# Kernel optimization log

Measured on AMD Instinct MI355X. Metric: run time of the kernel, lower is better.

Reference implementation:

```python
import jax, jax.numpy as jnp
import numpy as np

N = 50000
IN_F = 200
OUT_F = 200
NRELA = 200
E1 = 400000
E2 = 100000
ALPHA = 0.2  # leakyrelu slope


def setup_inputs() -> dict:
    key = jax.random.key(0)
    ks = jax.random.split(key, 9)
    xav = float(np.sqrt(2.0 / (OUT_F + 2 * IN_F + NRELA))) * 1.414
    return {
        "x": jax.random.normal(ks[0], (N, IN_F), dtype=jnp.float32),
        "edge": jax.random.randint(ks[1], (2, E1), 0, N, dtype=jnp.int32),
        "edge_embed": jax.random.normal(ks[2], (E1, NRELA), dtype=jnp.float32),
        "edge_list_nhop": jax.random.randint(ks[3], (2, E2), 0, N, dtype=jnp.int32),
        "edge_embed_nhop": jax.random.normal(ks[4], (E2, NRELA), dtype=jnp.float32),
        "a": jax.random.normal(ks[5], (OUT_F, 2 * IN_F + NRELA), dtype=jnp.float32) * xav,
        "a_2": jax.random.normal(ks[6], (1, OUT_F), dtype=jnp.float32) * float(np.sqrt(2.0 / (1 + OUT_F))) * 1.414,
        "mlp_w": jax.random.normal(ks[7], (1, OUT_F), dtype=jnp.float32) * float(np.sqrt(1.0 / OUT_F)),
        "mlp_b": jnp.zeros((1,), dtype=jnp.float32),
    }


def reference(x, edge, edge_embed, edge_list_nhop, edge_embed_nhop, a, a_2, mlp_w, mlp_b):
    # concat 1-hop and n-hop edges: e [2,E], emb [E,nrela]
    e = jnp.concatenate([edge, edge_list_nhop], axis=1)
    emb = jnp.concatenate([edge_embed, edge_embed_nhop], axis=0)
    src = e[0]
    dst = e[1]
    n_edges = emb.shape[0]
    # edge_h: [E, 2*in + nrela]
    edge_h = jnp.concatenate([x[src], x[dst], emb], axis=1)
    # edge_m = a @ edge_h.T, kept as [E, out]
    edge_m = edge_h @ a.T
    # powers = -leakyrelu(a_2 @ edge_m): [E]
    powers = -jax.nn.leaky_relu(edge_m @ a_2[0], ALPHA)
    # inline MLP: tanh(Linear(edge_m)) -> [E]
    y = jnp.tanh(edge_m @ mlp_w[0] + mlp_b[0])
    powers = powers * y / n_edges
    edge_e = jnp.exp(powers)  # [E]
    n = x.shape[0]
    # segment-sum over source nodes (sparse.sum over dim=1 of coo[src,dst,:])
    e_rowsum = jax.ops.segment_sum(edge_e, src, num_segments=n)[:, None]  # [N,1]
    e_rowsum = jnp.where(e_rowsum == 0.0, 1e-12, e_rowsum)
    # weighted scatter-add of edge messages
    edge_w = edge_e[:, None] * edge_m  # [E, out]
    h_prime = jax.ops.segment_sum(edge_w, src, num_segments=n)  # [N, out]
    h_prime = h_prime / e_rowsum
    return jax.nn.elu(h_prime)  # concat=True
```

## Files before the change

### kernel.cpp

```cpp
#include <hip/hip_runtime.h>
#include <math.h>

#define NN    50000
#define FDIM  200
#define E1N   400000
#define E2N   100000
#define EN    500000

typedef __attribute__((ext_vector_type(8))) short short8;
typedef __attribute__((ext_vector_type(4))) float f32x4;

#define VALL_OFF   0
#define WALL_OFF   608
#define SCAL_OFF   1216
#define XS_OFF     201216
#define RS_OFF     10201216
#define CNT_OFF    10251216
#define FILL_OFF   10301216
#define INCL_OFF   10351216
#define BSUM_OFF   10401216
#define SORT_OFF   10401472
#define XB_OFF     10901472
#define AB_OFF     15901472
#define TB_OFF     15961472

static __device__ __forceinline__ unsigned short f2bf(float f) {
    unsigned int u = __float_as_uint(f);
    unsigned int r = (u + 0x7fffu + ((u >> 16) & 1u)) >> 16;
    return (unsigned short)r;
}

__global__ void k_coeffs(const float* __restrict__ a, const float* __restrict__ a2,
                         const float* __restrict__ mlpw,
                         float* __restrict__ vall, float* __restrict__ wall) {
    int k = blockIdx.x * blockDim.x + threadIdx.x;
    if (k >= 600) return;
    float v = 0.f, w = 0.f;
    for (int o = 0; o < FDIM; ++o) {
        float av = a[o * 600 + k];
        v += a2[o] * av;
        w += mlpw[o] * av;
    }
    vall[k] = v;
    wall[k] = w;
}

__global__ __launch_bounds__(256) void k_node_scal(const float* __restrict__ x,
                                                   const float* __restrict__ vall,
                                                   const float* __restrict__ wall,
                                                   float* __restrict__ scal) {
    __shared__ float sv[1200];
    int tid = threadIdx.x;
    for (int i = tid; i < 1200; i += 256) sv[i] = (i < 600) ? vall[i] : wall[i - 600];
    __syncthreads();
    int lane = tid & 63;
    int n = blockIdx.x * 4 + (tid >> 6);
    float ps = 0.f, pd = 0.f, qs = 0.f, qd = 0.f;
    for (int k = lane; k < FDIM; k += 64) {
        float xv = x[(size_t)n * FDIM + k];
        ps += xv * sv[k];
        pd += xv * sv[200 + k];
        qs += xv * sv[600 + k];
        qd += xv * sv[800 + k];
    }
    #pragma unroll
    for (int off = 32; off > 0; off >>= 1) {
        ps += __shfl_xor(ps, off);
        pd += __shfl_xor(pd, off);
        qs += __shfl_xor(qs, off);
        qd += __shfl_xor(qd, off);
    }
    if (lane == 0) {
        float4 r = make_float4(ps, pd, qs, qd);
        *(float4*)(scal + (size_t)n * 4) = r;
    }
}

__global__ __launch_bounds__(256) void k_cvt(const float* __restrict__ src,
                                             unsigned short* __restrict__ dst, int n4) {
    int i = blockIdx.x * 256 + threadIdx.x;
    if (i >= n4) return;
    float4 v = *(const float4*)(src + (size_t)i * 4);
    ushort4 o;
    o.x = f2bf(v.x); o.y = f2bf(v.y); o.z = f2bf(v.z); o.w = f2bf(v.w);
    *(ushort4*)(dst + (size_t)i * 4) = o;
}

__global__ __launch_bounds__(256) void k_hist(const int* __restrict__ edge,
                                              const int* __restrict__ edgenh,
                                              int* __restrict__ counts) {
    int g = blockIdx.x * 256 + threadIdx.x;
    if (g >= EN) return;
    int s = (g < E1N) ? edge[g] : edgenh[g - E1N];
    atomicAdd(counts + s, 1);
}

__global__ __launch_bounds__(256) void k_scan1(const int* __restrict__ counts,
                                               int* __restrict__ incl,
                                               int* __restrict__ bsums) {
    __shared__ int tmp[256];
    int g = blockIdx.x * 256 + threadIdx.x;
    int v = (g < NN) ? counts[g] : 0;
    tmp[threadIdx.x] = v;
    __syncthreads();
    for (int off = 1; off < 256; off <<= 1) {
        int t = (threadIdx.x >= off) ? tmp[threadIdx.x - off] : 0;
        __syncthreads();
        tmp[threadIdx.x] += t;
        __syncthreads();
    }
    if (g < NN) incl[g] = tmp[threadIdx.x];
    if (threadIdx.x == 255) bsums[blockIdx.x] = tmp[255];
}

__global__ __launch_bounds__(256) void k_scan2(int* __restrict__ bsums, int nb) {
    __shared__ int tmp[256];
    int v = (threadIdx.x < nb) ? bsums[threadIdx.x] : 0;
    tmp[threadIdx.x] = v;
    __syncthreads();
    for (int off = 1; off < 256; off <<= 1) {
        int t = (threadIdx.x >= off) ? tmp[threadIdx.x - off] : 0;
        __syncthreads();
        tmp[threadIdx.x] += t;
        __syncthreads();
    }
    if (threadIdx.x < nb) bsums[threadIdx.x] = tmp[threadIdx.x] - v;
}

__global__ __launch_bounds__(256) void k_scan3(const int* __restrict__ counts,
                                               int* __restrict__ incl,
                                               const int* __restrict__ bsums) {
    int g = blockIdx.x * 256 + threadIdx.x;
    if (g >= NN) return;
    incl[g] = incl[g] - counts[g] + bsums[blockIdx.x];
}

__global__ __launch_bounds__(256) void k_scatter(const int* __restrict__ edge,
                                                 const int* __restrict__ edgenh,
                                                 const int* __restrict__ offs,
                                                 int* __restrict__ fill,
                                                 int* __restrict__ sorted) {
    int g = blockIdx.x * 256 + threadIdx.x;
    if (g >= EN) return;
    int s = (g < E1N) ? edge[g] : edgenh[g - E1N];
    int pos = offs[s] + atomicAdd(fill + s, 1);
    sorted[pos] = g;
}

__global__ __launch_bounds__(256) void k_csr(const int* __restrict__ sorted,
                                             const int* __restrict__ offs,
                                             const int* __restrict__ counts,
                                             const int* __restrict__ edge,
                                             const int* __restrict__ edgenh,
                                             const float* __restrict__ ee,
                                             const float* __restrict__ eenh,
                                             const float* __restrict__ x,
                                             const float* __restrict__ vall,
                                             const float* __restrict__ wall,
                                             const float* __restrict__ scal,
                                             const float* __restrict__ mlpb,
                                             float* __restrict__ rowsum,
                                             unsigned short* __restrict__ Tb) {
    int tid = threadIdx.x, lane = tid & 63;
    int n = blockIdx.x * 4 + (tid >> 6);
    float4 v3 = make_float4(0, 0, 0, 0), w3 = v3;
    if (lane < 50) {
        v3 = *(const float4*)(vall + 400 + lane * 4);
        w3 = *(const float4*)(wall + 400 + lane * 4);
    }
    float4 sc_n = *(const float4*)(scal + (size_t)n * 4);
    float mb = mlpb[0];
    int beg = offs[n], cnt = counts[n];
    float accx0 = 0, accx1 = 0, accx2 = 0, accx3 = 0;
    float acce0 = 0, acce1 = 0, acce2 = 0, acce3 = 0;
    float rs = 0.f;
    for (int i = 0; i < cnt; ++i) {
        int e = sorted[beg + i];
        int d;
        const float* erow;
        if (e < E1N) { d = edge[E1N + e]; erow = ee + (size_t)e * FDIM; }
        else { int e2 = e - E1N; d = edgenh[E2N + e2]; erow = eenh + (size_t)e2 * FDIM; }
        float4 ev = make_float4(0, 0, 0, 0), xv = ev;
        if (lane < 50) {
            ev = *(const float4*)(erow + lane * 4);
            xv = *(const float4*)(x + (size_t)d * FDIM + lane * 4);
        }
        float pe = ev.x * v3.x + ev.y * v3.y + ev.z * v3.z + ev.w * v3.w;
        float qe = ev.x * w3.x + ev.y * w3.y + ev.z * w3.z + ev.w * w3.w;
        #pragma unroll
        for (int off = 32; off > 0; off >>= 1) {
            pe += __shfl_xor(pe, off);
            qe += __shfl_xor(qe, off);
        }
        float4 sd = *(const float4*)(scal + (size_t)d * 4);
        float z1 = sc_n.x + sd.y + pe;
        float z2 = sc_n.z + sd.w + qe + mb;
        float l = z1 > 0.f ? z1 : 0.2f * z1;
        float wgt = expf((-l) * tanhf(z2) * (1.0f / (float)EN));
        rs += wgt;
        accx0 += wgt * xv.x; accx1 += wgt * xv.y; accx2 += wgt * xv.z; accx3 += wgt * xv.w;
        acce0 += wgt * ev.x; acce1 += wgt * ev.y; acce2 += wgt * ev.z; acce3 += wgt * ev.w;
    }
    if (lane == 0) rowsum[n] = rs;
    if (lane < 50) {
        ushort4 o1, o2;
        o1.x = f2bf(accx0); o1.y = f2bf(accx1); o1.z = f2bf(accx2); o1.w = f2bf(accx3);
        o2.x = f2bf(acce0); o2.y = f2bf(acce1); o2.z = f2bf(acce2); o2.w = f2bf(acce3);
        *(ushort4*)(Tb + (size_t)n * 400 + lane * 4) = o1;
        *(ushort4*)(Tb + (size_t)n * 400 + 200 + lane * 4) = o2;
    }
}

template <int KPAD, int KREAL, int LDA, int LDB, bool FINAL>
__global__ __launch_bounds__(256) void k_mfma(const unsigned short* __restrict__ A,
                                              const unsigned short* __restrict__ B,
                                              const float* __restrict__ Xs,
                                              const float* __restrict__ rowsum,
                                              float* __restrict__ C) {
    __shared__ unsigned short Al[64][40];
    __shared__ unsigned short Bl[64][40];
    int tid = threadIdx.x, w = tid >> 6, lane = tid & 63;
    int bx = blockIdx.x, by = blockIdx.y;
    f32x4 acc[4] = {};
    int r = tid >> 2, c = tid & 3;
    for (int k0 = 0; k0 < KPAD; k0 += 32) {
        int gk = k0 + c * 8;
        uint4 av = make_uint4(0, 0, 0, 0), bv = av;
        int arow = by * 64 + r;
        if (arow < NN && gk < KREAL)
            av = *(const uint4*)(A + (size_t)arow * LDA + gk);
        int brow = bx * 64 + r;
        if (brow < 200 && gk < KREAL)
            bv = *(const uint4*)(B + (size_t)brow * LDB + gk);
        *(uint4*)&Al[r][c * 8] = av;
        *(uint4*)&Bl[r][c * 8] = bv;
        __syncthreads();
        short8 af = *(short8*)&Al[w * 16 + (lane & 15)][(lane >> 4) * 8];
        #pragma unroll
        for (int ct = 0; ct < 4; ++ct) {
            short8 bf = *(short8*)&Bl[ct * 16 + (lane & 15)][(lane >> 4) * 8];
            acc[ct] = __builtin_amdgcn_mfma_f32_16x16x32_bf16(af, bf, acc[ct], 0, 0, 0);
        }
        __syncthreads();
    }
    #pragma unroll
    for (int ct = 0; ct < 4; ++ct) {
        #pragma unroll
        for (int rr = 0; rr < 4; ++rr) {
            int grow = by * 64 + w * 16 + (lane >> 4) * 4 + rr;
            int gcol = bx * 64 + ct * 16 + (lane & 15);
            if (grow < NN && gcol < 200) {
                float v = acc[ct][rr];
                if (FINAL) {
                    float rsv = rowsum[grow];
                    float o;
                    if (rsv == 0.f) o = 0.f;
                    else {
                        float h = Xs[(size_t)grow * 200 + gcol] + v / rsv;
                        o = h > 0.f ? h : expm1f(h);
                    }
                    C[(size_t)grow * 200 + gcol] = o;
                } else {
                    C[(size_t)grow * 200 + gcol] = v;
                }
            }
        }
    }
}

extern "C" void kernel_launch(void* const* d_in, const int* in_sizes, int n_in,
                              void* d_out, int out_size, void* d_ws, size_t ws_size,
                              hipStream_t stream) {
    const float* x      = (const float*)d_in[0];
    const int*   edge   = (const int*)d_in[1];
    const float* ee     = (const float*)d_in[2];
    const int*   edgenh = (const int*)d_in[3];
    const float* eenh   = (const float*)d_in[4];
    const float* a      = (const float*)d_in[5];
    const float* a2     = (const float*)d_in[6];
    const float* mlpw   = (const float*)d_in[7];
    const float* mlpb   = (const float*)d_in[8];

    float* ws = (float*)d_ws;
    float* vall   = ws + VALL_OFF;
    float* wall   = ws + WALL_OFF;
    float* scal   = ws + SCAL_OFF;
    float* Xs     = ws + XS_OFF;
    float* rowsum = ws + RS_OFF;
    int*   counts = (int*)(ws + CNT_OFF);
    int*   fill   = (int*)(ws + FILL_OFF);
    int*   incl   = (int*)(ws + INCL_OFF);
    int*   bsums  = (int*)(ws + BSUM_OFF);
    int*   sorted = (int*)(ws + SORT_OFF);
    unsigned short* xb = (unsigned short*)(ws + XB_OFF);
    unsigned short* ab = (unsigned short*)(ws + AB_OFF);
    unsigned short* Tb = (unsigned short*)(ws + TB_OFF);

    hipMemsetAsync(counts, 0, (size_t)(2 * NN) * sizeof(int), stream);

    k_coeffs<<<3, 256, 0, stream>>>(a, a2, mlpw, vall, wall);
    k_node_scal<<<NN / 4, 256, 0, stream>>>(x, vall, wall, scal);

    k_cvt<<<(NN * FDIM / 4 + 255) / 256, 256, 0, stream>>>(x, xb, NN * FDIM / 4);
    k_cvt<<<(200 * 600 / 4 + 255) / 256, 256, 0, stream>>>(a, ab, 200 * 600 / 4);

    k_hist<<<(EN + 255) / 256, 256, 0, stream>>>(edge, edgenh, counts);
    int nb = (NN + 255) / 256;
    k_scan1<<<nb, 256, 0, stream>>>(counts, incl, bsums);
    k_scan2<<<1, 256, 0, stream>>>(bsums, nb);
    k_scan3<<<nb, 256, 0, stream>>>(counts, incl, bsums);
    k_scatter<<<(EN + 255) / 256, 256, 0, stream>>>(edge, edgenh, incl, fill, sorted);

    dim3 gg(4, (NN + 63) / 64);
    k_mfma<224, 200, 200, 600, false><<<gg, 256, 0, stream>>>(xb, ab, nullptr, nullptr, Xs);

    k_csr<<<NN / 4, 256, 0, stream>>>(sorted, incl, counts, edge, edgenh, ee, eenh,
                                      x, vall, wall, scal, mlpb, rowsum, Tb);

    k_mfma<416, 400, 400, 600, true><<<gg, 256, 0, stream>>>(Tb, ab + 200, Xs, rowsum,
                                                             (float*)d_out);
}
```

Baseline: 821.9 us.

## Fuse two GEMMs into one K-concatenated GEMM and streamline CSR gather

Normalises the aggregated features by rowsum inside the CSR kernel, then computes the output with a single MFMA GEMM over the concatenated [x | T_src | T_emb] K dimension. This removes the intermediate fp32 Xs buffer and its write and read. Other changes: the bf16 conversion of x is fused into the node-scalar kernel, the CSR gather reads bf16 x, the destination is stored alongside the edge id in the sorted array, the next edge record is prefetched, and fast exp/rcp replace tanhf and expf. In exchange, the gathered neighbor features and normalised sums are rounded to bf16 and the fast transcendentals lose some accuracy.

```diff
diff --git a/kernel.cpp b/kernel.cpp
--- a/kernel.cpp
+++ b/kernel.cpp
@@ -13,21 +13,23 @@
 #define VALL_OFF   0
 #define WALL_OFF   608
 #define SCAL_OFF   1216
-#define XS_OFF     201216
-#define RS_OFF     10201216
-#define CNT_OFF    10251216
-#define FILL_OFF   10301216
-#define INCL_OFF   10351216
-#define BSUM_OFF   10401216
-#define SORT_OFF   10401472
-#define XB_OFF     10901472
-#define AB_OFF     15901472
-#define TB_OFF     15961472
+#define RS_OFF     201216
+#define CNT_OFF    251216
+#define FILL_OFF   301216
+#define INCL_OFF   351216
+#define BSUM_OFF   401216
+#define SORT_OFF   401472
+#define XB_OFF     1401472
+#define AB_OFF     6401472
+#define TSB_OFF    6461472
 
 static __device__ __forceinline__ unsigned short f2bf(float f) {
     unsigned int u = __float_as_uint(f);
     unsigned int r = (u + 0x7fffu + ((u >> 16) & 1u)) >> 16;
     return (unsigned short)r;
+}
+static __device__ __forceinline__ float bf2f(unsigned short s) {
+    return __uint_as_float((unsigned int)s << 16);
 }
 
 __global__ void k_coeffs(const float* __restrict__ a, const float* __restrict__ a2,
@@ -48,7 +50,8 @@
 __global__ __launch_bounds__(256) void k_node_scal(const float* __restrict__ x,
                                                    const float* __restrict__ vall,
                                                    const float* __restrict__ wall,
-                                                   float* __restrict__ scal) {
+                                                   float* __restrict__ scal,
+                                                   unsigned short* __restrict__ xb) {
     __shared__ float sv[1200];
     int tid = threadIdx.x;
     for (int i = tid; i < 1200; i += 256) sv[i] = (i < 600) ? vall[i] : wall[i - 600];
@@ -56,12 +59,19 @@
     int lane = tid & 63;
     int n = blockIdx.x * 4 + (tid >> 6);
     float ps = 0.f, pd = 0.f, qs = 0.f, qd = 0.f;
-    for (int k = lane; k < FDIM; k += 64) {
-        float xv = x[(size_t)n * FDIM + k];
-        ps += xv * sv[k];
-        pd += xv * sv[200 + k];
-        qs += xv * sv[600 + k];
-        qd += xv * sv[800 + k];
+    if (lane < 50) {
+        float4 xv = *(const float4*)(x + (size_t)n * FDIM + lane * 4);
+        float4 v1 = *(const float4*)(sv + lane * 4);
+        float4 v2 = *(const float4*)(sv + 200 + lane * 4);
+        float4 w1 = *(const float4*)(sv + 600 + lane * 4);
+        float4 w2 = *(const float4*)(sv + 800 + lane * 4);
+        ps = xv.x * v1.x + xv.y * v1.y + xv.z * v1.z + xv.w * v1.w;
+        pd = xv.x * v2.x + xv.y * v2.y + xv.z * v2.z + xv.w * v2.w;
+        qs = xv.x * w1.x + xv.y * w1.y + xv.z * w1.z + xv.w * w1.w;
+        qd = xv.x * w2.x + xv.y * w2.y + xv.z * w2.z + xv.w * w2.w;
+        ushort4 o;
+        o.x = f2bf(xv.x); o.y = f2bf(xv.y); o.z = f2bf(xv.z); o.w = f2bf(xv.w);
+        *(ushort4*)(xb + (size_t)n * FDIM + lane * 4) = o;
     }
     #pragma unroll
     for (int off = 32; off > 0; off >>= 1) {
@@ -129,38 +139,40 @@
 
 __global__ __launch_bounds__(256) void k_scan3(const int* __restrict__ counts,
                                                int* __restrict__ incl,
-                                               const int* __restrict__ bsums) {
+                                               const int* __restrict__ bsums,
+                                               int* __restrict__ fill) {
     int g = blockIdx.x * 256 + threadIdx.x;
     if (g >= NN) return;
-    incl[g] = incl[g] - counts[g] + bsums[blockIdx.x];
+    int v = incl[g] - counts[g] + bsums[blockIdx.x];
+    incl[g] = v;
+    fill[g] = v;
 }
 
 __global__ __launch_bounds__(256) void k_scatter(const int* __restrict__ edge,
                                                  const int* __restrict__ edgenh,
-                                                 const int* __restrict__ offs,
                                                  int* __restrict__ fill,
-                                                 int* __restrict__ sorted) {
+                                                 int2* __restrict__ sorted2) {
     int g = blockIdx.x * 256 + threadIdx.x;
     if (g >= EN) return;
-    int s = (g < E1N) ? edge[g] : edgenh[g - E1N];
-    int pos = offs[s] + atomicAdd(fill + s, 1);
-    sorted[pos] = g;
-}
-
-__global__ __launch_bounds__(256) void k_csr(const int* __restrict__ sorted,
+    int s, d;
+    if (g < E1N) { s = edge[g]; d = edge[E1N + g]; }
+    else { s = edgenh[g - E1N]; d = edgenh[E2N + (g - E1N)]; }
+    int pos = atomicAdd(fill + s, 1);
+    sorted2[pos] = make_int2(g, d);
+}
+
+__global__ __launch_bounds__(256) void k_csr(const int2* __restrict__ sorted2,
                                              const int* __restrict__ offs,
                                              const int* __restrict__ counts,
-                                             const int* __restrict__ edge,
-                                             const int* __restrict__ edgenh,
                                              const float* __restrict__ ee,
                                              const float* __restrict__ eenh,
-                                             const float* __restrict__ x,
+                                             const unsigned short* __restrict__ xb,
                                              const float* __restrict__ vall,
                                              const float* __restrict__ wall,
                                              const float* __restrict__ scal,
                                              const float* __restrict__ mlpb,
                                              float* __restrict__ rowsum,
-                                             unsigned short* __restrict__ Tb) {
+                                             unsigned short* __restrict__ Tsb) {
     int tid = threadIdx.x, lane = tid & 63;
     int n = blockIdx.x * 4 + (tid >> 6);
     float4 v3 = make_float4(0, 0, 0, 0), w3 = v3;
@@ -174,16 +186,17 @@
     float accx0 = 0, accx1 = 0, accx2 = 0, accx3 = 0;
     float acce0 = 0, acce1 = 0, acce2 = 0, acce3 = 0;
     float rs = 0.f;
+    int2 ed = (cnt > 0) ? sorted2[beg] : make_int2(0, 0);
     for (int i = 0; i < cnt; ++i) {
-        int e = sorted[beg + i];
-        int d;
-        const float* erow;
-        if (e < E1N) { d = edge[E1N + e]; erow = ee + (size_t)e * FDIM; }
-        else { int e2 = e - E1N; d = edgenh[E2N + e2]; erow = eenh + (size_t)e2 * FDIM; }
+        int2 ed_n = (i + 1 < cnt) ? sorted2[beg + i + 1] : ed;
+        int e = ed.x, d = ed.y;
+        const float* erow = (e < E1N) ? ee + (size_t)e * FDIM
+                                      : eenh + (size_t)(e - E1N) * FDIM;
         float4 ev = make_float4(0, 0, 0, 0), xv = ev;
         if (lane < 50) {
             ev = *(const float4*)(erow + lane * 4);
-            xv = *(const float4*)(x + (size_t)d * FDIM + lane * 4);
+            ushort4 xu = *(const ushort4*)(xb + (size_t)d * FDIM + lane * 4);
+            xv.x = bf2f(xu.x); xv.y = bf2f(xu.y); xv.z = bf2f(xu.z); xv.w = bf2f(xu.w);
         }
         float pe = ev.x * v3.x + ev.y * v3.y + ev.z * v3.z + ev.w * v3.w;
         float qe = ev.x * w3.x + ev.y * w3.y + ev.z * w3.z + ev.w * w3.w;
@@ -196,42 +209,55 @@
         float z1 = sc_n.x + sd.y + pe;
         float z2 = sc_n.z + sd.w + qe + mb;
         float l = z1 > 0.f ? z1 : 0.2f * z1;
-        float wgt = expf((-l) * tanhf(z2) * (1.0f / (float)EN));
+        float e2 = __expf(2.f * z2);
+        float t = 1.f - 2.f * __builtin_amdgcn_rcpf(e2 + 1.f);
+        float wgt = __expf(l * t * (-1.f / (float)EN));
         rs += wgt;
         accx0 += wgt * xv.x; accx1 += wgt * xv.y; accx2 += wgt * xv.z; accx3 += wgt * xv.w;
         acce0 += wgt * ev.x; acce1 += wgt * ev.y; acce2 += wgt * ev.z; acce3 += wgt * ev.w;
+        ed = ed_n;
     }
     if (lane == 0) rowsum[n] = rs;
+    float inv = (cnt > 0) ? __builtin_amdgcn_rcpf(rs) : 0.f;
     if (lane < 50) {
         ushort4 o1, o2;
-        o1.x = f2bf(accx0); o1.y = f2bf(accx1); o1.z = f2bf(accx2); o1.w = f2bf(accx3);
-        o2.x = f2bf(acce0); o2.y = f2bf(acce1); o2.z = f2bf(acce2); o2.w = f2bf(acce3);
-        *(ushort4*)(Tb + (size_t)n * 400 + lane * 4) = o1;
-        *(ushort4*)(Tb + (size_t)n * 400 + 200 + lane * 4) = o2;
-    }
-}
-
-template <int KPAD, int KREAL, int LDA, int LDB, bool FINAL>
-__global__ __launch_bounds__(256) void k_mfma(const unsigned short* __restrict__ A,
-                                              const unsigned short* __restrict__ B,
-                                              const float* __restrict__ Xs,
-                                              const float* __restrict__ rowsum,
-                                              float* __restrict__ C) {
+        o1.x = f2bf(accx0 * inv); o1.y = f2bf(accx1 * inv);
+        o1.z = f2bf(accx2 * inv); o1.w = f2bf(accx3 * inv);
+        o2.x = f2bf(acce0 * inv); o2.y = f2bf(acce1 * inv);
+        o2.z = f2bf(acce2 * inv); o2.w = f2bf(acce3 * inv);
+        *(ushort4*)(Tsb + (size_t)n * 400 + lane * 4) = o1;
+        *(ushort4*)(Tsb + (size_t)n * 400 + 200 + lane * 4) = o2;
+    }
+}
+
+__global__ __launch_bounds__(256) void k_gemm_fused(const unsigned short* __restrict__ xb,
+                                                    const unsigned short* __restrict__ tsb,
+                                                    const unsigned short* __restrict__ ab,
+                                                    const float* __restrict__ rowsum,
+                                                    float* __restrict__ out) {
     __shared__ unsigned short Al[64][40];
     __shared__ unsigned short Bl[64][40];
     int tid = threadIdx.x, w = tid >> 6, lane = tid & 63;
     int bx = blockIdx.x, by = blockIdx.y;
     f32x4 acc[4] = {};
     int r = tid >> 2, c = tid & 3;
-    for (int k0 = 0; k0 < KPAD; k0 += 32) {
+    int arow = by * 64 + r;
+    int brow = bx * 64 + r;
+    bool inA = arow < NN;
+    bool inB = brow < 200;
+    const unsigned short* aPx = xb + (size_t)arow * 200;
+    const unsigned short* aPt = tsb + (size_t)arow * 400;
+    const unsigned short* bP = ab + (size_t)brow * 600;
+    for (int k0 = 0; k0 < 640; k0 += 32) {
         int gk = k0 + c * 8;
         uint4 av = make_uint4(0, 0, 0, 0), bv = av;
-        int arow = by * 64 + r;
-        if (arow < NN && gk < KREAL)
-            av = *(const uint4*)(A + (size_t)arow * LDA + gk);
-        int brow = bx * 64 + r;
-        if (brow < 200 && gk < KREAL)
-            bv = *(const uint4*)(B + (size_t)brow * LDB + gk);
+        if (gk < 200) {
+            if (inA) av = *(const uint4*)(aPx + gk);
+            if (inB) bv = *(const uint4*)(bP + gk);
+        } else if (gk >= 224 && gk < 624) {
+            if (inA) av = *(const uint4*)(aPt + (gk - 224));
+            if (inB) bv = *(const uint4*)(bP + gk - 24);
+        }
         *(uint4*)&Al[r][c * 8] = av;
         *(uint4*)&Bl[r][c * 8] = bv;
         __syncthreads();
@@ -250,19 +276,10 @@
             int grow = by * 64 + w * 16 + (lane >> 4) * 4 + rr;
             int gcol = bx * 64 + ct * 16 + (lane & 15);
             if (grow < NN && gcol < 200) {
-                float v = acc[ct][rr];
-                if (FINAL) {
-                    float rsv = rowsum[grow];
-                    float o;
-                    if (rsv == 0.f) o = 0.f;
-                    else {
-                        float h = Xs[(size_t)grow * 200 + gcol] + v / rsv;
-                        o = h > 0.f ? h : expm1f(h);
-                    }
-                    C[(size_t)grow * 200 + gcol] = o;
-                } else {
-                    C[(size_t)grow * 200 + gcol] = v;
-                }
+                float rsv = rowsum[grow];
+                float h = acc[ct][rr];
+                float o = (rsv == 0.f) ? 0.f : (h > 0.f ? h : expm1f(h));
+                out[(size_t)grow * 200 + gcol] = o;
             }
         }
     }
@@ -285,38 +302,32 @@
     float* vall   = ws + VALL_OFF;
     float* wall   = ws + WALL_OFF;
     float* scal   = ws + SCAL_OFF;
-    float* Xs     = ws + XS_OFF;
     float* rowsum = ws + RS_OFF;
     int*   counts = (int*)(ws + CNT_OFF);
     int*   fill   = (int*)(ws + FILL_OFF);
     int*   incl   = (int*)(ws + INCL_OFF);
     int*   bsums  = (int*)(ws + BSUM_OFF);
-    int*   sorted = (int*)(ws + SORT_OFF);
-    unsigned short* xb = (unsigned short*)(ws + XB_OFF);
-    unsigned short* ab = (unsigned short*)(ws + AB_OFF);
-    unsigned short* Tb = (unsigned short*)(ws + TB_OFF);
+    int2*  sorted2 = (int2*)(ws + SORT_OFF);
+    unsigned short* xb  = (unsigned short*)(ws + XB_OFF);
+    unsigned short* ab  = (unsigned short*)(ws + AB_OFF);
+    unsigned short* tsb = (unsigned short*)(ws + TSB_OFF);
 
     hipMemsetAsync(counts, 0, (size_t)(2 * NN) * sizeof(int), stream);
 
     k_coeffs<<<3, 256, 0, stream>>>(a, a2, mlpw, vall, wall);
-    k_node_scal<<<NN / 4, 256, 0, stream>>>(x, vall, wall, scal);
-
-    k_cvt<<<(NN * FDIM / 4 + 255) / 256, 256, 0, stream>>>(x, xb, NN * FDIM / 4);
+    k_node_scal<<<NN / 4, 256, 0, stream>>>(x, vall, wall, scal, xb);
     k_cvt<<<(200 * 600 / 4 + 255) / 256, 256, 0, stream>>>(a, ab, 200 * 600 / 4);
 
     k_hist<<<(EN + 255) / 256, 256, 0, stream>>>(edge, edgenh, counts);
     int nb = (NN + 255) / 256;
     k_scan1<<<nb, 256, 0, stream>>>(counts, incl, bsums);
     k_scan2<<<1, 256, 0, stream>>>(bsums, nb);
-    k_scan3<<<nb, 256, 0, stream>>>(counts, incl, bsums);
-    k_scatter<<<(EN + 255) / 256, 256, 0, stream>>>(edge, edgenh, incl, fill, sorted);
+    k_scan3<<<nb, 256, 0, stream>>>(counts, incl, bsums, fill);
+    k_scatter<<<(EN + 255) / 256, 256, 0, stream>>>(edge, edgenh, fill, sorted2);
+
+    k_csr<<<NN / 4, 256, 0, stream>>>(sorted2, incl, counts, ee, eenh, xb,
+                                      vall, wall, scal, mlpb, rowsum, tsb);
 
     dim3 gg(4, (NN + 63) / 64);
-    k_mfma<224, 200, 200, 600, false><<<gg, 256, 0, stream>>>(xb, ab, nullptr, nullptr, Xs);
-
-    k_csr<<<NN / 4, 256, 0, stream>>>(sorted, incl, counts, edge, edgenh, ee, eenh,
-                                      x, vall, wall, scal, mlpb, rowsum, Tb);
-
-    k_mfma<416, 400, 400, 600, true><<<gg, 256, 0, stream>>>(Tb, ab + 200, Xs, rowsum,
-                                                             (float*)d_out);
-}
+    k_gemm_fused<<<gg, 256, 0, stream>>>(xb, tsb, ab, rowsum, (float*)d_out);
+}
```

Result: faster. 746.4 us (-9.2%).
